# Kernel tuning notes

Hardware: AMD Instinct MI355X
Metric: run time of the kernel (lower is better)

The kernel has to match this reference:

```python
import jax, jax.numpy as jnp
import numpy as np

B, S, HH, WW = 256, 384, 12, 16
D = HH * WW          # 192, LSTM input dim
H = 100              # hidden_dim
C = 250              # output_dim (N_CLASSES)


def setup_inputs() -> dict:
    key = jax.random.key(0)
    k1, k2, k3, k4 = jax.random.split(key, 4)
    x = jax.random.normal(k1, (B, S, HH, WW), dtype=jnp.float32)
    # Glorot-ish scaling to keep the recurrence numerically tame
    W = jax.random.normal(k2, (D, 4 * H), dtype=jnp.float32) / np.sqrt(D)
    U = jax.random.normal(k3, (H, 4 * H), dtype=jnp.float32) / np.sqrt(H)
    b = jnp.zeros((4 * H,), dtype=jnp.float32)
    Wd = jax.random.normal(k4, (H, C), dtype=jnp.float32) / np.sqrt(H)
    bd = jnp.zeros((C,), dtype=jnp.float32)
    return {"x": x, "W": W, "U": U, "b": b, "Wd": Wd, "bd": bd}


def _lstm_last_hidden(x3, W, U, b):
    # x3: [B, S, D]. Keras gate order: i, f, c(g), o.
    pre = jnp.einsum('bsd,dk->sbk', x3, W) + b  # time-major [S, B, 4H]
    h0 = jnp.zeros((x3.shape[0], H), dtype=x3.dtype)
    c0 = jnp.zeros_like(h0)

    def step(carry, xt):
        h, c = carry
        z = xt + h @ U                      # [B, 4H]
        i = jax.nn.sigmoid(z[:, 0 * H:1 * H])
        f = jax.nn.sigmoid(z[:, 1 * H:2 * H])
        g = jnp.tanh(z[:, 2 * H:3 * H])
        o = jax.nn.sigmoid(z[:, 3 * H:4 * H])
        c_new = f * c + i * g
        h_new = o * jnp.tanh(c_new)
        return (h_new, c_new), None

    (hT, _), _ = jax.lax.scan(step, (h0, c0), pre)
    return hT  # [B, H] == out[:, -1, :] since return_sequences last step = final state


def reference(x, W, U, b, Wd, bd):
    b_, s_, hh_, ww_ = x.shape
    x3 = x.reshape(b_, s_, hh_ * ww_)
    hT = _lstm_last_hidden(x3, W, U, b)
    # Dropout layers are identity at inference (training=False)
    return hT @ Wd + bd  # [B, C] logits
```

## Files before the change

### kernel.cpp

```cpp
#include <hip/hip_runtime.h>
#include <cstdint>
#include <cstddef>

#define S_LEN 384
#define BATCH 256
#define DIM   192
#define HID   100
#define G4    400
#define NCLS  250

#define LOG2E  1.4426950408889634f
#define LOG2E2 2.8853900817779268f

typedef float    f32x4   __attribute__((ext_vector_type(4)));
typedef short    bf16x8  __attribute__((ext_vector_type(8)));
typedef _Float16 half2_t __attribute__((ext_vector_type(2)));
typedef _Float16 f16x4   __attribute__((ext_vector_type(4)));
typedef _Float16 f16x8   __attribute__((ext_vector_type(8)));

static __device__ __forceinline__ unsigned short f2bf(float f) {
    unsigned u = __float_as_uint(f);
    return (unsigned short)((u + 0x7FFFu + ((u >> 16) & 1u)) >> 16);
}

template<int CTRL>
static __device__ __forceinline__ float fdpp(float x) {
    return __int_as_float(
        __builtin_amdgcn_mov_dpp(__float_as_int(x), CTRL, 0xF, 0xF, true));
}
#define DPP_X1 0xB1

__global__ void prep(const float* __restrict__ W, const float* __restrict__ U,
                     unsigned short* __restrict__ Wt, half2_t* __restrict__ Ut2b)
{
    int bid = blockIdx.x;
    if (bid < 300) {
        int i = bid * 256 + threadIdx.x;
        if (i >= G4 * DIM) return;
        int k = i / DIM, d = i - k * DIM;
        Wt[i] = f2bf(W[(size_t)d * G4 + k]);
    } else {
        int i = (bid - 300) * 256 + threadIdx.x;
        if (i >= 20800) return;
        int n    = i / 208;
        int rem  = i - n * 208;
        int p    = rem / 104;
        int rem2 = rem - p * 104;
        int gi   = rem2 / 26;
        int r    = rem2 - gi * 26;
        int g    = (gi < 2) ? (2 * p + gi) : (2 * (1 - p) + (gi - 2));
        int col  = g * HID + n;
        int j0   = 52 * p + 2 * r;
        half2_t v;
        v.x = (_Float16)(j0     < HID ? U[(size_t)j0       * G4 + col] : 0.0f);
        v.y = (_Float16)(j0 + 1 < HID ? U[(size_t)(j0 + 1) * G4 + col] : 0.0f);
        Ut2b[i] = v;
    }
}

__global__ __launch_bounds__(256, 2)
void gemm_pre(const float* __restrict__ x, const unsigned short* __restrict__ Wt,
              const float* __restrict__ bias, _Float16* __restrict__ preh,
              int s_start, int chunk)
{
    __shared__ unsigned int xs[64 * 100];
    __shared__ unsigned int wsh[400 * 20];

    const int t    = threadIdx.x;
    const int lane = t & 63;
    const int w    = t >> 6;
    const int nsb  = chunk >> 6;
    const int b    = blockIdx.x / nsb;
    const int sblk = blockIdx.x - b * nsb;
    const float* __restrict__ xb = x + ((size_t)b * S_LEN + s_start + sblk * 64) * DIM;

#pragma unroll
    for (int r = 0; r < 12; ++r) {
        int i = t + r * 256;
        int row = i / 48, c4 = i - row * 48;
        float4 v = ((const float4*)(xb + (size_t)row * DIM))[c4];
        xs[row * 100 + c4 * 2]     = (unsigned)f2bf(v.x) | ((unsigned)f2bf(v.y) << 16);
        xs[row * 100 + c4 * 2 + 1] = (unsigned)f2bf(v.z) | ((unsigned)f2bf(v.w) << 16);
    }

    const int m = lane & 15, q = lane >> 4;

    float bv[25];
#pragma unroll
    for (int ct = 0; ct < 25; ++ct) bv[ct] = bias[ct * 16 + m];

    f32x4 acc[25];
#pragma unroll
    for (int ct = 0; ct < 25; ++ct) acc[ct] = (f32x4){0.f, 0.f, 0.f, 0.f};

    for (int dc = 0; dc < 6; ++dc) {
        if (dc) __syncthreads();
#pragma unroll
        for (int r = 0; r < 7; ++r) {
            int i = t + r * 256;
            if (i < 1600) {
                int k = i >> 2, u4 = i & 3;
                uint4 v = *(const uint4*)(Wt + (size_t)k * DIM + dc * 32 + u4 * 8);
                *(uint4*)(wsh + k * 20 + u4 * 4) = v;
            }
        }
        __syncthreads();

        const unsigned short* xp = (const unsigned short*)xs
                                   + (16 * w + m) * 200 + dc * 32 + q * 8;
        bf16x8 af = *(const bf16x8*)xp;
#pragma unroll
        for (int ct = 0; ct < 25; ++ct) {
            const unsigned short* bp = (const unsigned short*)wsh
                                       + (ct * 16 + m) * 40 + q * 8;
            bf16x8 bf = *(const bf16x8*)bp;
            acc[ct] = __builtin_amdgcn_mfma_f32_16x16x32_bf16(af, bf, acc[ct], 0, 0, 0);
        }
    }

    _Float16* __restrict__ pb = preh + (size_t)b * G4 * chunk + (size_t)sblk * 64
                                + 16 * w + q * 4;
#pragma unroll
    for (int ct = 0; ct < 25; ++ct) {
        f16x4 v;
        v[0] = (_Float16)(acc[ct][0] + bv[ct]);
        v[1] = (_Float16)(acc[ct][1] + bv[ct]);
        v[2] = (_Float16)(acc[ct][2] + bv[ct]);
        v[3] = (_Float16)(acc[ct][3] + bv[ct]);
        *(f16x4*)(pb + (size_t)(ct * 16 + m) * chunk) = v;
    }
}

__global__ __launch_bounds__(256)
void lstm_scan(const _Float16* __restrict__ preh, const half2_t* __restrict__ Ut2b,
               const float* __restrict__ Wd, const float* __restrict__ bd,
               float* __restrict__ out, float* __restrict__ state,
               int nsteps, int first, int last)
{
    __shared__ __align__(16) _Float16 h2[2][112];
    __shared__ __align__(16) float hf32[HID];

    const int b  = blockIdx.x;
    const int t  = threadIdx.x;
    const int p  = t & 1;
    const int nr = t >> 1;
    const int n  = (nr < HID) ? nr : HID - 1;
    const bool active = (nr < HID);
    const int slot = (n < 52) ? n : (56 + n - 52);

    half2_t Uc[4][26];
#pragma unroll
    for (int gi = 0; gi < 4; ++gi) {
        const half2_t* up = Ut2b + (size_t)((n * 2 + p) * 4 + gi) * 26;
#pragma unroll
        for (int r = 0; r < 26; ++r) Uc[gi][r] = up[r];
    }

    if (t < 224) ((_Float16*)h2)[t] = (_Float16)0.f;
    float c;
    if (first) {
        c = 0.f;
        __syncthreads();
    } else {
        c = state[BATCH * HID + b * HID + n];
        __syncthreads();
        if (t < HID) h2[0][(t < 52) ? t : (56 + t - 52)] = (_Float16)state[b * HID + t];
        __syncthreads();
    }

    const _Float16* __restrict__ zpA = preh + ((size_t)b * G4 + (2 * p)     * HID + n) * nsteps;
    const _Float16* __restrict__ zpB = preh + ((size_t)b * G4 + (2 * p + 1) * HID + n) * nsteps;

    const float scaleA = p ? -LOG2E2 : -LOG2E;
    const float AactA  = p ? 2.0f : 1.0f;
    const float BactA  = p ? -1.0f : 0.0f;

    float hn_last = 0.f;

    auto step = [&](float zAk, float zBk, int cur) {
        const _Float16* hb = &h2[cur][p * 56];
        f16x8  g0 = *(const f16x8*)(hb);
        f16x8  g1 = *(const f16x8*)(hb + 8);
        f16x8  g2 = *(const f16x8*)(hb + 16);
        f16x8  g3 = *(const f16x8*)(hb + 24);
        f16x8  g4 = *(const f16x8*)(hb + 32);
        f16x8  g5 = *(const f16x8*)(hb + 40);
        f16x4  g6 = *(const f16x4*)(hb + 48);
        half2_t hp[26];
        hp[0]  = __builtin_shufflevector(g0, g0, 0, 1);
        hp[1]  = __builtin_shufflevector(g0, g0, 2, 3);
        hp[2]  = __builtin_shufflevector(g0, g0, 4, 5);
        hp[3]  = __builtin_shufflevector(g0, g0, 6, 7);
        hp[4]  = __builtin_shufflevector(g1, g1, 0, 1);
        hp[5]  = __builtin_shufflevector(g1, g1, 2, 3);
        hp[6]  = __builtin_shufflevector(g1, g1, 4, 5);
        hp[7]  = __builtin_shufflevector(g1, g1, 6, 7);
        hp[8]  = __builtin_shufflevector(g2, g2, 0, 1);
        hp[9]  = __builtin_shufflevector(g2, g2, 2, 3);
        hp[10] = __builtin_shufflevector(g2, g2, 4, 5);
        hp[11] = __builtin_shufflevector(g2, g2, 6, 7);
        hp[12] = __builtin_shufflevector(g3, g3, 0, 1);
        hp[13] = __builtin_shufflevector(g3, g3, 2, 3);
        hp[14] = __builtin_shufflevector(g3, g3, 4, 5);
        hp[15] = __builtin_shufflevector(g3, g3, 6, 7);
        hp[16] = __builtin_shufflevector(g4, g4, 0, 1);
        hp[17] = __builtin_shufflevector(g4, g4, 2, 3);
        hp[18] = __builtin_shufflevector(g4, g4, 4, 5);
        hp[19] = __builtin_shufflevector(g4, g4, 6, 7);
        hp[20] = __builtin_shufflevector(g5, g5, 0, 1);
        hp[21] = __builtin_shufflevector(g5, g5, 2, 3);
        hp[22] = __builtin_shufflevector(g5, g5, 4, 5);
        hp[23] = __builtin_shufflevector(g5, g5, 6, 7);
        hp[24] = __builtin_shufflevector(g6, g6, 0, 1);
        hp[25] = __builtin_shufflevector(g6, g6, 2, 3);

        float qa0 = 0.f, qa1 = 0.f, qa2 = 0.f, qa3 = 0.f;
        float qb0 = 0.f, qb1 = 0.f, qb2 = 0.f, qb3 = 0.f;
#pragma unroll
        for (int r = 0; r < 13; ++r) {
            qa0 = __builtin_amdgcn_fdot2(Uc[0][r], hp[r], qa0, false);
            qa1 = __builtin_amdgcn_fdot2(Uc[1][r], hp[r], qa1, false);
            qa2 = __builtin_amdgcn_fdot2(Uc[2][r], hp[r], qa2, false);
            qa3 = __builtin_amdgcn_fdot2(Uc[3][r], hp[r], qa3, false);
        }
#pragma unroll
        for (int r = 13; r < 26; ++r) {
            qb0 = __builtin_amdgcn_fdot2(Uc[0][r], hp[r], qb0, false);
            qb1 = __builtin_amdgcn_fdot2(Uc[1][r], hp[r], qb1, false);
            qb2 = __builtin_amdgcn_fdot2(Uc[2][r], hp[r], qb2, false);
            qb3 = __builtin_amdgcn_fdot2(Uc[3][r], hp[r], qb3, false);
        }
        float a0 = qa0 + qb0;
        float a1 = qa1 + qb1;
        float a2 = qa2 + qb2;
        float a3 = qa3 + qb3;

        float aA = a0 + fdpp<DPP_X1>(a2) + zAk;
        float aB = a1 + fdpp<DPP_X1>(a3) + zBk;

        float vA = fmaf(AactA,
                        __builtin_amdgcn_rcpf(1.0f + __builtin_amdgcn_exp2f(scaleA * aA)),
                        BactA);
        float vB = __builtin_amdgcn_rcpf(1.0f + __builtin_amdgcn_exp2f(-LOG2E * aB));
        float gA = fdpp<DPP_X1>(vA);
        float gB = fdpp<DPP_X1>(vB);

        c = fmaf(vB, c, vA * gA);
        float tc = fmaf(2.0f,
                        __builtin_amdgcn_rcpf(1.0f + __builtin_amdgcn_exp2f(-LOG2E2 * c)),
                        -1.0f);
        float hn = gB * tc;
        if (p == 0 && active) h2[cur ^ 1][slot] = (_Float16)hn;
        hn_last = hn;
        __syncthreads();
    };

    for (int s8 = 0; s8 < nsteps; s8 += 8) {
        f16x8 zva = *(const f16x8*)(zpA + s8);
        f16x8 zvb = *(const f16x8*)(zpB + s8);
#pragma unroll
        for (int k = 0; k < 8; ++k)
            step((float)zva[k], (float)zvb[k], k & 1);
    }

    if (last) {
        if (p == 0 && active) hf32[n] = hn_last;
        __syncthreads();
        if (t < NCLS) {
            float acc2 = bd[t];
            const float4* h4 = (const float4*)hf32;
#pragma unroll 5
            for (int j4 = 0; j4 < 25; ++j4) {
                float4 hv = h4[j4];
                acc2 = fmaf(hv.x, Wd[(size_t)(4 * j4 + 0) * NCLS + t], acc2);
                acc2 = fmaf(hv.y, Wd[(size_t)(4 * j4 + 1) * NCLS + t], acc2);
                acc2 = fmaf(hv.z, Wd[(size_t)(4 * j4 + 2) * NCLS + t], acc2);
                acc2 = fmaf(hv.w, Wd[(size_t)(4 * j4 + 3) * NCLS + t], acc2);
            }
            out[(size_t)b * NCLS + t] = acc2;
        }
    } else {
        if (p == 0 && active) {
            state[b * HID + n] = hn_last;
            state[BATCH * HID + b * HID + n] = c;
        }
    }
}

extern "C" void kernel_launch(void* const* d_in, const int* in_sizes, int n_in,
                              void* d_out, int out_size, void* d_ws, size_t ws_size,
                              hipStream_t stream)
{
    const float* x    = (const float*)d_in[0];
    const float* W    = (const float*)d_in[1];
    const float* U    = (const float*)d_in[2];
    const float* bias = (const float*)d_in[3];
    const float* Wd   = (const float*)d_in[4];
    const float* bd   = (const float*)d_in[5];
    float* out = (float*)d_out;

    const size_t fixed_dw = 51200 + 20800 + 38400;
    int chunk = 64;
    if      (ws_size >= (fixed_dw + (size_t)384 * 51200) * 4) chunk = 384;
    else if (ws_size >= (fixed_dw + (size_t)192 * 51200) * 4) chunk = 192;
    const int nchunks = S_LEN / chunk;

    unsigned int* wsb = (unsigned int*)d_ws;
    float*          state = (float*)wsb;
    half2_t*        Ut2b  = (half2_t*)(wsb + 51200);
    unsigned short* Wt    = (unsigned short*)(wsb + 72000);
    _Float16*       preh  = (_Float16*)(wsb + 110400);

    prep<<<382, 256, 0, stream>>>(W, U, Wt, Ut2b);

    for (int ci = 0; ci < nchunks; ++ci) {
        const int s0 = ci * chunk;
        gemm_pre<<<BATCH * (chunk >> 6), 256, 0, stream>>>(x, Wt, bias, preh, s0, chunk);
        lstm_scan<<<BATCH, 256, 0, stream>>>(preh, Ut2b, Wd, bd, out, state,
                                             chunk, ci == 0 ? 1 : 0,
                                             ci == nchunks - 1 ? 1 : 0);
    }
}
```

Baseline: 323.8 us.

## Split LSTM recurrence across four lanes per hidden unit with 512-thread blocks

The scan kernel now assigns four threads per hidden unit instead of two. Each thread computes one gate over a quarter of h and reduces partials with DPP swaps, then broadcasts the gate values with DPP quad broadcasts. This halves the serial dot-product chain per step on the latency-bound recurrence. The U layout in prep and the h shared-memory layout are reorganised to match, and the preactivation vector for the next 8 steps is prefetched. In exchange, blocks are twice as large (512 threads), so each barrier synchronises more waves, and there are extra cross-lane ops per step.

```diff
diff --git a/kernel.cpp b/kernel.cpp
--- a/kernel.cpp
+++ b/kernel.cpp
@@ -29,9 +29,14 @@
         __builtin_amdgcn_mov_dpp(__float_as_int(x), CTRL, 0xF, 0xF, true));
 }
 #define DPP_X1 0xB1
+#define DPP_X2 0x4E
+#define DPP_B0 0x00
+#define DPP_B1 0x55
+#define DPP_B2 0xAA
+#define DPP_B3 0xFF
 
 __global__ void prep(const float* __restrict__ W, const float* __restrict__ U,
-                     unsigned short* __restrict__ Wt, half2_t* __restrict__ Ut2b)
+                     unsigned short* __restrict__ Wt, half2_t* __restrict__ Ut4)
 {
     int bid = blockIdx.x;
     if (bid < 300) {
@@ -44,17 +49,16 @@
         if (i >= 20800) return;
         int n    = i / 208;
         int rem  = i - n * 208;
-        int p    = rem / 104;
-        int rem2 = rem - p * 104;
-        int gi   = rem2 / 26;
-        int r    = rem2 - gi * 26;
-        int g    = (gi < 2) ? (2 * p + gi) : (2 * (1 - p) + (gi - 2));
-        int col  = g * HID + n;
-        int j0   = 52 * p + 2 * r;
+        int q    = rem / 52;
+        int rem2 = rem - q * 52;
+        int m    = rem2 / 13;
+        int r    = rem2 - m * 13;
+        int col  = (q ^ m) * HID + n;
+        int j0   = 26 * q + 2 * r;
         half2_t v;
         v.x = (_Float16)(j0     < HID ? U[(size_t)j0       * G4 + col] : 0.0f);
         v.y = (_Float16)(j0 + 1 < HID ? U[(size_t)(j0 + 1) * G4 + col] : 0.0f);
-        Ut2b[i] = v;
+        Ut4[i] = v;
     }
 }
 
@@ -131,32 +135,32 @@
     }
 }
 
-__global__ __launch_bounds__(256)
-void lstm_scan(const _Float16* __restrict__ preh, const half2_t* __restrict__ Ut2b,
+__global__ __launch_bounds__(512, 2)
+void lstm_scan(const _Float16* __restrict__ preh, const half2_t* __restrict__ Ut4,
                const float* __restrict__ Wd, const float* __restrict__ bd,
                float* __restrict__ out, float* __restrict__ state,
                int nsteps, int first, int last)
 {
-    __shared__ __align__(16) _Float16 h2[2][112];
+    __shared__ __align__(16) _Float16 h2[2][4][40];
     __shared__ __align__(16) float hf32[HID];
 
     const int b  = blockIdx.x;
     const int t  = threadIdx.x;
-    const int p  = t & 1;
-    const int nr = t >> 1;
-    const int n  = (nr < HID) ? nr : HID - 1;
+    const int q  = t & 3;
+    const int nr = t >> 2;
     const bool active = (nr < HID);
-    const int slot = (n < 52) ? n : (56 + n - 52);
-
-    half2_t Uc[4][26];
-#pragma unroll
-    for (int gi = 0; gi < 4; ++gi) {
-        const half2_t* up = Ut2b + (size_t)((n * 2 + p) * 4 + gi) * 26;
-#pragma unroll
-        for (int r = 0; r < 26; ++r) Uc[gi][r] = up[r];
-    }
-
-    if (t < 224) ((_Float16*)h2)[t] = (_Float16)0.f;
+    const int n  = active ? nr : HID - 1;
+    const int wq = n / 26, wi = n - wq * 26;
+
+    half2_t Uc[4][13];
+#pragma unroll
+    for (int m = 0; m < 4; ++m) {
+        const half2_t* up = Ut4 + (size_t)((n * 4 + q) * 4 + m) * 13;
+#pragma unroll
+        for (int r = 0; r < 13; ++r) Uc[m][r] = up[r];
+    }
+
+    if (t < 320) ((_Float16*)h2)[t] = (_Float16)0.f;
     float c;
     if (first) {
         c = 0.f;
@@ -164,29 +168,25 @@
     } else {
         c = state[BATCH * HID + b * HID + n];
         __syncthreads();
-        if (t < HID) h2[0][(t < 52) ? t : (56 + t - 52)] = (_Float16)state[b * HID + t];
-        __syncthreads();
-    }
-
-    const _Float16* __restrict__ zpA = preh + ((size_t)b * G4 + (2 * p)     * HID + n) * nsteps;
-    const _Float16* __restrict__ zpB = preh + ((size_t)b * G4 + (2 * p + 1) * HID + n) * nsteps;
-
-    const float scaleA = p ? -LOG2E2 : -LOG2E;
-    const float AactA  = p ? 2.0f : 1.0f;
-    const float BactA  = p ? -1.0f : 0.0f;
+        if (t < HID) h2[0][t / 26][t - (t / 26) * 26] = (_Float16)state[b * HID + t];
+        __syncthreads();
+    }
+
+    const _Float16* __restrict__ zp = preh + ((size_t)b * G4 + q * HID + n) * nsteps;
+
+    const float scale = (q == 2) ? -LOG2E2 : -LOG2E;
+    const float Aact  = (q == 2) ? 2.0f : 1.0f;
+    const float Bact  = (q == 2) ? -1.0f : 0.0f;
 
     float hn_last = 0.f;
 
-    auto step = [&](float zAk, float zBk, int cur) {
-        const _Float16* hb = &h2[cur][p * 56];
-        f16x8  g0 = *(const f16x8*)(hb);
-        f16x8  g1 = *(const f16x8*)(hb + 8);
-        f16x8  g2 = *(const f16x8*)(hb + 16);
-        f16x8  g3 = *(const f16x8*)(hb + 24);
-        f16x8  g4 = *(const f16x8*)(hb + 32);
-        f16x8  g5 = *(const f16x8*)(hb + 40);
-        f16x4  g6 = *(const f16x4*)(hb + 48);
-        half2_t hp[26];
+    auto step = [&](float zk, int cur) {
+        const _Float16* hb = &h2[cur][q][0];
+        f16x8   g0 = *(const f16x8*)(hb);
+        f16x8   g1 = *(const f16x8*)(hb + 8);
+        f16x8   g2 = *(const f16x8*)(hb + 16);
+        half2_t g3 = *(const half2_t*)(hb + 24);
+        half2_t hp[13];
         hp[0]  = __builtin_shufflevector(g0, g0, 0, 1);
         hp[1]  = __builtin_shufflevector(g0, g0, 2, 3);
         hp[2]  = __builtin_shufflevector(g0, g0, 4, 5);
@@ -199,72 +199,51 @@
         hp[9]  = __builtin_shufflevector(g2, g2, 2, 3);
         hp[10] = __builtin_shufflevector(g2, g2, 4, 5);
         hp[11] = __builtin_shufflevector(g2, g2, 6, 7);
-        hp[12] = __builtin_shufflevector(g3, g3, 0, 1);
-        hp[13] = __builtin_shufflevector(g3, g3, 2, 3);
-        hp[14] = __builtin_shufflevector(g3, g3, 4, 5);
-        hp[15] = __builtin_shufflevector(g3, g3, 6, 7);
-        hp[16] = __builtin_shufflevector(g4, g4, 0, 1);
-        hp[17] = __builtin_shufflevector(g4, g4, 2, 3);
-        hp[18] = __builtin_shufflevector(g4, g4, 4, 5);
-        hp[19] = __builtin_shufflevector(g4, g4, 6, 7);
-        hp[20] = __builtin_shufflevector(g5, g5, 0, 1);
-        hp[21] = __builtin_shufflevector(g5, g5, 2, 3);
-        hp[22] = __builtin_shufflevector(g5, g5, 4, 5);
-        hp[23] = __builtin_shufflevector(g5, g5, 6, 7);
-        hp[24] = __builtin_shufflevector(g6, g6, 0, 1);
-        hp[25] = __builtin_shufflevector(g6, g6, 2, 3);
-
-        float qa0 = 0.f, qa1 = 0.f, qa2 = 0.f, qa3 = 0.f;
-        float qb0 = 0.f, qb1 = 0.f, qb2 = 0.f, qb3 = 0.f;
+        hp[12] = g3;
+
+        float p0 = 0.f, p1 = 0.f, p2 = 0.f, p3 = 0.f;
 #pragma unroll
         for (int r = 0; r < 13; ++r) {
-            qa0 = __builtin_amdgcn_fdot2(Uc[0][r], hp[r], qa0, false);
-            qa1 = __builtin_amdgcn_fdot2(Uc[1][r], hp[r], qa1, false);
-            qa2 = __builtin_amdgcn_fdot2(Uc[2][r], hp[r], qa2, false);
-            qa3 = __builtin_amdgcn_fdot2(Uc[3][r], hp[r], qa3, false);
-        }
-#pragma unroll
-        for (int r = 13; r < 26; ++r) {
-            qb0 = __builtin_amdgcn_fdot2(Uc[0][r], hp[r], qb0, false);
-            qb1 = __builtin_amdgcn_fdot2(Uc[1][r], hp[r], qb1, false);
-            qb2 = __builtin_amdgcn_fdot2(Uc[2][r], hp[r], qb2, false);
-            qb3 = __builtin_amdgcn_fdot2(Uc[3][r], hp[r], qb3, false);
-        }
-        float a0 = qa0 + qb0;
-        float a1 = qa1 + qb1;
-        float a2 = qa2 + qb2;
-        float a3 = qa3 + qb3;
-
-        float aA = a0 + fdpp<DPP_X1>(a2) + zAk;
-        float aB = a1 + fdpp<DPP_X1>(a3) + zBk;
-
-        float vA = fmaf(AactA,
-                        __builtin_amdgcn_rcpf(1.0f + __builtin_amdgcn_exp2f(scaleA * aA)),
-                        BactA);
-        float vB = __builtin_amdgcn_rcpf(1.0f + __builtin_amdgcn_exp2f(-LOG2E * aB));
-        float gA = fdpp<DPP_X1>(vA);
-        float gB = fdpp<DPP_X1>(vB);
-
-        c = fmaf(vB, c, vA * gA);
+            p0 = __builtin_amdgcn_fdot2(Uc[0][r], hp[r], p0, false);
+            p1 = __builtin_amdgcn_fdot2(Uc[1][r], hp[r], p1, false);
+            p2 = __builtin_amdgcn_fdot2(Uc[2][r], hp[r], p2, false);
+            p3 = __builtin_amdgcn_fdot2(Uc[3][r], hp[r], p3, false);
+        }
+        float s0 = p0 + fdpp<DPP_X1>(p1);
+        float s2 = p2 + fdpp<DPP_X1>(p3);
+        float a  = s0 + fdpp<DPP_X2>(s2) + zk;
+
+        float v = fmaf(Aact,
+                       __builtin_amdgcn_rcpf(1.0f + __builtin_amdgcn_exp2f(scale * a)),
+                       Bact);
+
+        float bi = fdpp<DPP_B0>(v);
+        float bf = fdpp<DPP_B1>(v);
+        float bg = fdpp<DPP_B2>(v);
+        float bo = fdpp<DPP_B3>(v);
+
+        c = fmaf(bf, c, bi * bg);
         float tc = fmaf(2.0f,
                         __builtin_amdgcn_rcpf(1.0f + __builtin_amdgcn_exp2f(-LOG2E2 * c)),
                         -1.0f);
-        float hn = gB * tc;
-        if (p == 0 && active) h2[cur ^ 1][slot] = (_Float16)hn;
+        float hn = bo * tc;
+        if (q == 0 && active) h2[cur ^ 1][wq][wi] = (_Float16)hn;
         hn_last = hn;
         __syncthreads();
     };
 
+    f16x8 zv = *(const f16x8*)(zp);
     for (int s8 = 0; s8 < nsteps; s8 += 8) {
-        f16x8 zva = *(const f16x8*)(zpA + s8);
-        f16x8 zvb = *(const f16x8*)(zpB + s8);
+        f16x8 zvn = zv;
+        if (s8 + 8 < nsteps) zvn = *(const f16x8*)(zp + s8 + 8);
 #pragma unroll
         for (int k = 0; k < 8; ++k)
-            step((float)zva[k], (float)zvb[k], k & 1);
+            step((float)zv[k], k & 1);
+        zv = zvn;
     }
 
     if (last) {
-        if (p == 0 && active) hf32[n] = hn_last;
+        if (q == 0 && active) hf32[n] = hn_last;
         __syncthreads();
         if (t < NCLS) {
             float acc2 = bd[t];
@@ -280,7 +259,7 @@
             out[(size_t)b * NCLS + t] = acc2;
         }
     } else {
-        if (p == 0 && active) {
+        if (q == 0 && active) {
             state[b * HID + n] = hn_last;
             state[BATCH * HID + b * HID + n] = c;
         }
@@ -307,16 +286,16 @@
 
     unsigned int* wsb = (unsigned int*)d_ws;
     float*          state = (float*)wsb;
-    half2_t*        Ut2b  = (half2_t*)(wsb + 51200);
+    half2_t*        Ut4   = (half2_t*)(wsb + 51200);
     unsigned short* Wt    = (unsigned short*)(wsb + 72000);
     _Float16*       preh  = (_Float16*)(wsb + 110400);
 
-    prep<<<382, 256, 0, stream>>>(W, U, Wt, Ut2b);
+    prep<<<382, 256, 0, stream>>>(W, U, Wt, Ut4);
 
     for (int ci = 0; ci < nchunks; ++ci) {
         const int s0 = ci * chunk;
         gemm_pre<<<BATCH * (chunk >> 6), 256, 0, stream>>>(x, Wt, bias, preh, s0, chunk);
-        lstm_scan<<<BATCH, 256, 0, stream>>>(preh, Ut2b, Wd, bd, out, state,
+        lstm_scan<<<BATCH, 512, 0, stream>>>(preh, Ut4, Wd, bd, out, state,
                                              chunk, ci == 0 ? 1 : 0,
                                              ci == nchunks - 1 ? 1 : 0);
     }
```

Result: no change. 322.8 us (-0.3%).
